# Optimization experiments

Measured on AMD Instinct MI355X. Metric: run time of the kernel, lower is better.

## Reference

```python
import jax, jax.numpy as jnp
import numpy as np

B, N, F_IN, F_OUT = 16, 2048, 512, 512


def setup_inputs() -> dict:
    key = jax.random.key(0)
    k1, k2, k3 = jax.random.split(key, 3)
    x = jax.random.normal(k1, (B, N, F_IN), dtype=jnp.float32)
    adj = jax.random.uniform(k2, (N, N), dtype=jnp.float32)
    # Kaiming uniform fan_out: bound = sqrt(6 / fan_out)
    bound = np.sqrt(6.0 / F_OUT)
    weight = jax.random.uniform(k3, (F_IN, F_OUT), dtype=jnp.float32,
                                minval=-bound, maxval=bound)
    bias = jnp.zeros((F_OUT,), dtype=jnp.float32)
    return {"x": x, "adj": adj, "weight": weight, "bias": bias}


def reference(x, adj, weight, bias):
    # Symmetric degree normalization: D^{-1/2} A D^{-1/2}
    deg = adj.sum(axis=1)                                   # [N]
    deg_inv_sqrt = jnp.where(deg > 0, jax.lax.rsqrt(deg), 0.0)
    # row/column rescale instead of diag matmuls (same math, O(N^2))
    norm_adj = adj * deg_inv_sqrt[:, None] * deg_inv_sqrt[None, :]
    support = jnp.einsum('bni,io->bno', x, weight)          # [B,N,F_OUT]
    output = jnp.einsum('nm,bmo->bno', norm_adj, support)   # [B,N,F_OUT]
    return output + bias
```

## Files before the change

### kernel.cpp

```cpp
#include <hip/hip_runtime.h>
#include <stdint.h>

typedef __attribute__((ext_vector_type(8))) __bf16 bf16x8;
typedef __attribute__((ext_vector_type(4))) float f32x4;
typedef unsigned short u16;

__device__ __forceinline__ u16 f2bf(float f) {
  unsigned u = __builtin_bit_cast(unsigned, f);
  unsigned r = 0x7FFFu + ((u >> 16) & 1u);
  return (u16)((u + r) >> 16);
}

__device__ __forceinline__ void gload16(const void* g, void* l) {
  __builtin_amdgcn_global_load_lds(
      (__attribute__((address_space(1))) void*)(g),
      (__attribute__((address_space(3))) void*)(l),
      16, 0, 0);
}

__global__ void row_deg_k(const float* __restrict__ adj, float* __restrict__ dis, int N) {
  int row = blockIdx.x;
  const float4* a = (const float4*)(adj + (size_t)row * N);
  float s = 0.f;
  for (int j = threadIdx.x; j < N / 4; j += 256) {
    float4 v = a[j];
    s += v.x + v.y + v.z + v.w;
  }
#pragma unroll
  for (int off = 32; off > 0; off >>= 1) s += __shfl_down(s, off, 64);
  __shared__ float wsum[4];
  if ((threadIdx.x & 63) == 0) wsum[threadIdx.x >> 6] = s;
  __syncthreads();
  if (threadIdx.x == 0) {
    float t = wsum[0] + wsum[1] + wsum[2] + wsum[3];
    dis[row] = (t > 0.f) ? (1.0f / sqrtf(t)) : 0.f;
  }
}

__global__ void conv_bf16_k(const float* __restrict__ in, u16* __restrict__ o, int n4) {
  int i = blockIdx.x * 256 + threadIdx.x;
  if (i >= n4) return;
  float4 v = ((const float4*)in)[i];
  ushort4 u;
  u.x = f2bf(v.x); u.y = f2bf(v.y); u.z = f2bf(v.z); u.w = f2bf(v.w);
  ((ushort4*)o)[i] = u;
}

__global__ void conv_wt_k(const float* __restrict__ w, u16* __restrict__ wt) {
  int idx = blockIdx.x * 256 + threadIdx.x;
  int i = idx >> 9, o = idx & 511;
  wt[o * 512 + i] = f2bf(w[idx]);
}

__global__ void make_nadj_k(const float* __restrict__ adj, const float* __restrict__ dis,
                            u16* __restrict__ o, int N) {
  int idx = blockIdx.x * 256 + threadIdx.x;
  int i = idx >> 9;
  int j4 = (idx & 511) * 4;
  float di = dis[i];
  float4 a = ((const float4*)adj)[idx];
  ushort4 u;
  u.x = f2bf(a.x * di * dis[j4 + 0]);
  u.y = f2bf(a.y * di * dis[j4 + 1]);
  u.z = f2bf(a.z * di * dis[j4 + 2]);
  u.w = f2bf(a.w * di * dis[j4 + 3]);
  ((ushort4*)o)[idx] = u;
}

template <int EPI>
__launch_bounds__(512, 2)
__global__ void gemm256_k(const u16* __restrict__ A, int lda,
                          const u16* __restrict__ Bt, int ldb,
                          void* __restrict__ Cv, int ldc,
                          const float* __restrict__ bias, int K,
                          int nMT, int nNT, size_t zBt, size_t zC) {
  __shared__ __align__(16) u16 lds[65536];

  const int tid = threadIdx.x;
  const int lane = tid & 63;
  const int wid = tid >> 6;
  const int wr = wid >> 2;
  const int wc = wid & 3;

  const int flat = blockIdx.x;
  const int wg = (flat & 7) * ((int)gridDim.x >> 3) + (flat >> 3);
  const int m_t = wg % nMT;
  const int rest = wg / nMT;
  const int n_t = rest % nNT;
  const int b = rest / nNT;
  const int rowBase = m_t * 256;
  const int colBase = n_t * 256;
  const u16* Bb = Bt + (size_t)b * zBt;

  const int lr = tid >> 3;
  const int kkl = (tid & 7) * 8;
  const int kswz = kkl ^ ((lr & 7) << 3);
  const u16* gA = A + (size_t)(rowBase + lr) * lda + kswz;
  const u16* gB = Bb + (size_t)(colBase + lr) * ldb + kswz;
  u16* lA = lds + lr * 64 + kkl;
  u16* lB = lds + 32768 + lr * 64 + kkl;

  const int fr = lane & 15;
  const int rswz = (lane & 7) << 3;
  const int kp0 = ((lane >> 4) * 8) ^ rswz;
  const int kp1 = (32 | ((lane >> 4) * 8)) ^ rswz;
  const u16* fA = lds + (wr * 128 + fr) * 64;
  const u16* fB = lds + 32768 + (wc * 64 + fr) * 64;

  f32x4 acc[8][4] = {};

  const int NT = K >> 6;

#define STAGE_ALL(d, t)                                                              \
  _Pragma("unroll") for (int r4 = 0; r4 < 4; ++r4) {                                 \
    gload16(gA + (size_t)(r4 * 64) * lda + (size_t)(t) * 64,                         \
            lA + (d) * 16384 + r4 * 4096);                                           \
    gload16(gB + (size_t)(r4 * 64) * ldb + (size_t)(t) * 64,                         \
            lB + (d) * 16384 + r4 * 4096);                                           \
  }

  STAGE_ALL(0, 0);
  __syncthreads();

  for (int t = 0; t < NT; ++t) {
    const int c = t & 1;
    const int cn = c ^ 1;
    const int tn = (t + 1 < NT) ? t + 1 : NT - 1;

    STAGE_ALL(cn, tn);
    __builtin_amdgcn_sched_barrier(0);

    bf16x8 a0[8], a1[8], b0[4], b1[4];
#pragma unroll
    for (int m = 0; m < 8; ++m) {
      a0[m] = *(const bf16x8*)(fA + c * 16384 + m * 1024 + kp0);
      a1[m] = *(const bf16x8*)(fA + c * 16384 + m * 1024 + kp1);
    }
#pragma unroll
    for (int n = 0; n < 4; ++n) {
      b0[n] = *(const bf16x8*)(fB + c * 16384 + n * 1024 + kp0);
      b1[n] = *(const bf16x8*)(fB + c * 16384 + n * 1024 + kp1);
    }
#pragma unroll
    for (int m = 0; m < 8; ++m)
#pragma unroll
      for (int n = 0; n < 4; ++n)
        acc[m][n] = __builtin_amdgcn_mfma_f32_16x16x32_bf16(a0[m], b0[n], acc[m][n], 0, 0, 0);
#pragma unroll
    for (int m = 0; m < 8; ++m)
#pragma unroll
      for (int n = 0; n < 4; ++n)
        acc[m][n] = __builtin_amdgcn_mfma_f32_16x16x32_bf16(a1[m], b1[n], acc[m][n], 0, 0, 0);

    __syncthreads();
  }

  if (EPI == 0) {
    u16* C = (u16*)Cv;
#pragma unroll
    for (int m = 0; m < 8; ++m) {
      const int r = rowBase + wr * 128 + m * 16 + (lane >> 4) * 4;
#pragma unroll
      for (int n = 0; n < 4; ++n) {
        const int cc = colBase + wc * 64 + n * 16 + (lane & 15);
        ushort4 v;
        v.x = f2bf(acc[m][n][0]);
        v.y = f2bf(acc[m][n][1]);
        v.z = f2bf(acc[m][n][2]);
        v.w = f2bf(acc[m][n][3]);
        *reinterpret_cast<ushort4*>(&C[(size_t)cc * ldc + r]) = v;
      }
    }
  } else {
    float* C = (float*)Cv + (size_t)b * zC;
#pragma unroll
    for (int n = 0; n < 4; ++n) {
      const int cc = colBase + wc * 64 + n * 16 + (lane & 15);
      const float bv = bias[cc];
#pragma unroll
      for (int m = 0; m < 8; ++m) {
        const int r = rowBase + wr * 128 + m * 16 + (lane >> 4) * 4;
#pragma unroll
        for (int j = 0; j < 4; ++j)
          C[(size_t)(r + j) * ldc + cc] = acc[m][n][j] + bv;
      }
    }
  }
#undef STAGE_ALL
}

extern "C" void kernel_launch(void* const* d_in, const int* in_sizes, int n_in,
                              void* d_out, int out_size, void* d_ws, size_t ws_size,
                              hipStream_t stream) {
  const int B = 16, N = 2048, FIN = 512, FOUT = 512;
  const float* x    = (const float*)d_in[0];
  const float* adj  = (const float*)d_in[1];
  const float* w    = (const float*)d_in[2];
  const float* bias = (const float*)d_in[3];
  float* out = (float*)d_out;
  char* ws = (char*)d_ws;

  float* dis = (float*)ws;
  u16* wt    = (u16*)(ws + 8192);
  u16* nadj  = (u16*)(ws + 532480);
  u16* xb    = (u16*)(ws + 8921088);
  u16* st    = (u16*)(ws + 42475520);

  row_deg_k<<<N, 256, 0, stream>>>(adj, dis, N);
  conv_bf16_k<<<(B * N * FIN / 4 + 255) / 256, 256, 0, stream>>>(x, xb, B * N * FIN / 4);
  conv_wt_k<<<(FIN * FOUT) / 256, 256, 0, stream>>>(w, wt);
  make_nadj_k<<<(N * N / 4) / 256, 256, 0, stream>>>(adj, dis, nadj, N);

  gemm256_k<0><<<dim3(256), 512, 0, stream>>>(
      xb, FIN, wt, FIN, st, B * N, nullptr, FIN, 128, 2, 0, 0);

  gemm256_k<1><<<dim3(256), 512, 0, stream>>>(
      nadj, N, st, B * N, out, FOUT, bias, N, 8, 2,
      (size_t)N, (size_t)N * FOUT);
}
```

Baseline: 124.6 us.

## Fuse x fp32-to-bf16 conversion into first GEMM and retile second GEMM

The separate x-to-bf16 conversion kernel is removed. The first GEMM now loads fp32 x through registers, converts it with the hardware bf16 conversion, and writes swizzled tiles to LDS, which saves a full write and re-read of the bf16 copy of x. The second GEMM uses 128-row tiles with single-buffered, smaller LDS, twice as many blocks, and higher occupancy (launch bounds 512,4). The cost is that it drops the double-buffered prefetch, so it now relies on occupancy to hide load latency.

```diff
diff --git a/kernel.cpp b/kernel.cpp
--- a/kernel.cpp
+++ b/kernel.cpp
@@ -1,4 +1,5 @@
 #include <hip/hip_runtime.h>
+#include <hip/hip_bf16.h>
 #include <stdint.h>
 
 typedef __attribute__((ext_vector_type(8))) __bf16 bf16x8;
@@ -9,6 +10,11 @@
   unsigned u = __builtin_bit_cast(unsigned, f);
   unsigned r = 0x7FFFu + ((u >> 16) & 1u);
   return (u16)((u + r) >> 16);
+}
+
+__device__ __forceinline__ u16 f2bf_hw(float f) {
+  __hip_bfloat16 h = __float2bfloat16(f);
+  return __builtin_bit_cast(u16, h);
 }
 
 __device__ __forceinline__ void gload16(const void* g, void* l) {
@@ -35,15 +41,6 @@
     float t = wsum[0] + wsum[1] + wsum[2] + wsum[3];
     dis[row] = (t > 0.f) ? (1.0f / sqrtf(t)) : 0.f;
   }
-}
-
-__global__ void conv_bf16_k(const float* __restrict__ in, u16* __restrict__ o, int n4) {
-  int i = blockIdx.x * 256 + threadIdx.x;
-  if (i >= n4) return;
-  float4 v = ((const float4*)in)[i];
-  ushort4 u;
-  u.x = f2bf(v.x); u.y = f2bf(v.y); u.z = f2bf(v.z); u.w = f2bf(v.w);
-  ((ushort4*)o)[i] = u;
 }
 
 __global__ void conv_wt_k(const float* __restrict__ w, u16* __restrict__ wt) {
@@ -67,13 +64,10 @@
   ((ushort4*)o)[idx] = u;
 }
 
-template <int EPI>
 __launch_bounds__(512, 2)
-__global__ void gemm256_k(const u16* __restrict__ A, int lda,
-                          const u16* __restrict__ Bt, int ldb,
-                          void* __restrict__ Cv, int ldc,
-                          const float* __restrict__ bias, int K,
-                          int nMT, int nNT, size_t zBt, size_t zC) {
+__global__ void gemm1_xw_k(const float* __restrict__ X,
+                           const u16* __restrict__ Wt,
+                           u16* __restrict__ Ct, int M) {
   __shared__ __align__(16) u16 lds[65536];
 
   const int tid = threadIdx.x;
@@ -83,12 +77,136 @@
   const int wc = wid & 3;
 
   const int flat = blockIdx.x;
-  const int wg = (flat & 7) * ((int)gridDim.x >> 3) + (flat >> 3);
+  const int wg = (flat & 7) * 32 + (flat >> 3);
+  const int m_t = wg & 127;
+  const int n_t = wg >> 7;
+  const int rowBase = m_t * 256;
+  const int colBase = n_t * 256;
+
+  const int lr = tid >> 3;
+  const int kkl = (tid & 7) * 8;
+  const int s = (lr & 7) << 3;
+  const int kswz = kkl ^ s;
+  const float* gX = X + (size_t)(rowBase + lr) * 512 + kkl;
+  const u16* gB = Wt + (size_t)(colBase + lr) * 512 + kswz;
+  u16* lAsw = lds + lr * 64 + kswz;
+  u16* lB = lds + 32768 + lr * 64 + kkl;
+
+  const int fr = lane & 15;
+  const int rswz = (lane & 7) << 3;
+  const int kp0 = ((lane >> 4) * 8) ^ rswz;
+  const int kp1 = (32 | ((lane >> 4) * 8)) ^ rswz;
+  const u16* fA = lds + (wr * 128 + fr) * 64;
+  const u16* fB = lds + 32768 + (wc * 64 + fr) * 64;
+
+  f32x4 acc[8][4] = {};
+  f32x4 xv[4][2];
+
+  const int NT = 8;
+
+#define LOADX(t)                                                                     \
+  _Pragma("unroll") for (int r4 = 0; r4 < 4; ++r4) {                                 \
+    xv[r4][0] = *(const f32x4*)(gX + (size_t)(r4 * 64) * 512 + (t) * 64);            \
+    xv[r4][1] = *(const f32x4*)(gX + (size_t)(r4 * 64) * 512 + (t) * 64 + 4);        \
+  }
+
+#define STAGE_B1(d, t)                                                               \
+  _Pragma("unroll") for (int r4 = 0; r4 < 4; ++r4)                                   \
+    gload16(gB + (size_t)(r4 * 64) * 512 + (size_t)(t) * 64,                         \
+            lB + (d) * 16384 + r4 * 4096);
+
+#define WRITE_A(d)                                                                   \
+  _Pragma("unroll") for (int r4 = 0; r4 < 4; ++r4) {                                 \
+    bf16x8 v;                                                                        \
+    _Pragma("unroll") for (int i = 0; i < 4; ++i) {                                  \
+      v[i] = __builtin_bit_cast(__bf16, f2bf_hw(xv[r4][0][i]));                      \
+      v[4 + i] = __builtin_bit_cast(__bf16, f2bf_hw(xv[r4][1][i]));                  \
+    }                                                                                \
+    *(bf16x8*)(lAsw + (d) * 16384 + r4 * 4096) = v;                                  \
+  }
+
+  LOADX(0);
+  STAGE_B1(0, 0);
+  WRITE_A(0);
+  __syncthreads();
+
+  for (int t = 0; t < NT; ++t) {
+    const int c = t & 1;
+    const int cn = c ^ 1;
+    const int tn = (t + 1 < NT) ? t + 1 : NT - 1;
+
+    LOADX(tn);
+    STAGE_B1(cn, tn);
+    __builtin_amdgcn_sched_barrier(0);
+
+    bf16x8 a0[8], a1[8], b0[4], b1[4];
+#pragma unroll
+    for (int m = 0; m < 8; ++m) {
+      a0[m] = *(const bf16x8*)(fA + c * 16384 + m * 1024 + kp0);
+      a1[m] = *(const bf16x8*)(fA + c * 16384 + m * 1024 + kp1);
+    }
+#pragma unroll
+    for (int n = 0; n < 4; ++n) {
+      b0[n] = *(const bf16x8*)(fB + c * 16384 + n * 1024 + kp0);
+      b1[n] = *(const bf16x8*)(fB + c * 16384 + n * 1024 + kp1);
+    }
+#pragma unroll
+    for (int m = 0; m < 8; ++m)
+#pragma unroll
+      for (int n = 0; n < 4; ++n)
+        acc[m][n] = __builtin_amdgcn_mfma_f32_16x16x32_bf16(a0[m], b0[n], acc[m][n], 0, 0, 0);
+#pragma unroll
+    for (int m = 0; m < 8; ++m)
+#pragma unroll
+      for (int n = 0; n < 4; ++n)
+        acc[m][n] = __builtin_amdgcn_mfma_f32_16x16x32_bf16(a1[m], b1[n], acc[m][n], 0, 0, 0);
+
+    __builtin_amdgcn_sched_barrier(0);
+    WRITE_A(cn);
+    __syncthreads();
+  }
+
+#pragma unroll
+  for (int m = 0; m < 8; ++m) {
+    const int r = rowBase + wr * 128 + m * 16 + (lane >> 4) * 4;
+#pragma unroll
+    for (int n = 0; n < 4; ++n) {
+      const int cc = colBase + wc * 64 + n * 16 + (lane & 15);
+      ushort4 v;
+      v.x = f2bf(acc[m][n][0]);
+      v.y = f2bf(acc[m][n][1]);
+      v.z = f2bf(acc[m][n][2]);
+      v.w = f2bf(acc[m][n][3]);
+      *reinterpret_cast<ushort4*>(&Ct[(size_t)cc * M + r]) = v;
+    }
+  }
+#undef LOADX
+#undef STAGE_B1
+#undef WRITE_A
+}
+
+__launch_bounds__(512, 4)
+__global__ void gemm2b_k(const u16* __restrict__ A, int lda,
+                         const u16* __restrict__ Bt, int ldb,
+                         float* __restrict__ C, int ldc,
+                         const float* __restrict__ bias, int K,
+                         int nMT, int nNT, size_t zBt, size_t zC) {
+  __shared__ __align__(16) u16 lds[24576];
+
+  const int tid = threadIdx.x;
+  const int lane = tid & 63;
+  const int wid = tid >> 6;
+  const int wr = wid >> 2;
+  const int wc = wid & 3;
+
+  const int flat = blockIdx.x;
+  const int cpx = (int)gridDim.x >> 3;
+  const int wg = (flat & 7) * cpx + (flat >> 3);
   const int m_t = wg % nMT;
   const int rest = wg / nMT;
   const int n_t = rest % nNT;
   const int b = rest / nNT;
-  const int rowBase = m_t * 256;
+  const int rowBase = m_t * 128;
   const int colBase = n_t * 256;
   const u16* Bb = Bt + (size_t)b * zBt;
 
@@ -98,95 +216,62 @@
   const u16* gA = A + (size_t)(rowBase + lr) * lda + kswz;
   const u16* gB = Bb + (size_t)(colBase + lr) * ldb + kswz;
   u16* lA = lds + lr * 64 + kkl;
-  u16* lB = lds + 32768 + lr * 64 + kkl;
+  u16* lB = lds + 8192 + lr * 64 + kkl;
 
   const int fr = lane & 15;
   const int rswz = (lane & 7) << 3;
   const int kp0 = ((lane >> 4) * 8) ^ rswz;
   const int kp1 = (32 | ((lane >> 4) * 8)) ^ rswz;
-  const u16* fA = lds + (wr * 128 + fr) * 64;
-  const u16* fB = lds + 32768 + (wc * 64 + fr) * 64;
-
-  f32x4 acc[8][4] = {};
-
+  const u16* fA = lds + (wr * 64 + fr) * 64;
+  const u16* fB = lds + 8192 + (wc * 64 + fr) * 64;
+
+  f32x4 acc[4][4] = {};
   const int NT = K >> 6;
 
-#define STAGE_ALL(d, t)                                                              \
-  _Pragma("unroll") for (int r4 = 0; r4 < 4; ++r4) {                                 \
-    gload16(gA + (size_t)(r4 * 64) * lda + (size_t)(t) * 64,                         \
-            lA + (d) * 16384 + r4 * 4096);                                           \
-    gload16(gB + (size_t)(r4 * 64) * ldb + (size_t)(t) * 64,                         \
-            lB + (d) * 16384 + r4 * 4096);                                           \
-  }
-
-  STAGE_ALL(0, 0);
-  __syncthreads();
-
   for (int t = 0; t < NT; ++t) {
-    const int c = t & 1;
-    const int cn = c ^ 1;
-    const int tn = (t + 1 < NT) ? t + 1 : NT - 1;
-
-    STAGE_ALL(cn, tn);
-    __builtin_amdgcn_sched_barrier(0);
-
-    bf16x8 a0[8], a1[8], b0[4], b1[4];
-#pragma unroll
-    for (int m = 0; m < 8; ++m) {
-      a0[m] = *(const bf16x8*)(fA + c * 16384 + m * 1024 + kp0);
-      a1[m] = *(const bf16x8*)(fA + c * 16384 + m * 1024 + kp1);
+    gload16(gA + (size_t)t * 64, lA);
+    gload16(gA + (size_t)64 * lda + (size_t)t * 64, lA + 4096);
+#pragma unroll
+    for (int r4 = 0; r4 < 4; ++r4)
+      gload16(gB + (size_t)(r4 * 64) * ldb + (size_t)t * 64, lB + r4 * 4096);
+    __syncthreads();
+
+    bf16x8 a[4], bb[4];
+#pragma unroll
+    for (int m = 0; m < 4; ++m) a[m] = *(const bf16x8*)(fA + m * 1024 + kp0);
+#pragma unroll
+    for (int n = 0; n < 4; ++n) bb[n] = *(const bf16x8*)(fB + n * 1024 + kp0);
+#pragma unroll
+    for (int m = 0; m < 4; ++m)
+#pragma unroll
+      for (int n = 0; n < 4; ++n)
+        acc[m][n] = __builtin_amdgcn_mfma_f32_16x16x32_bf16(a[m], bb[n], acc[m][n], 0, 0, 0);
+#pragma unroll
+    for (int m = 0; m < 4; ++m) a[m] = *(const bf16x8*)(fA + m * 1024 + kp1);
+#pragma unroll
+    for (int n = 0; n < 4; ++n) bb[n] = *(const bf16x8*)(fB + n * 1024 + kp1);
+#pragma unroll
+    for (int m = 0; m < 4; ++m)
+#pragma unroll
+      for (int n = 0; n < 4; ++n)
+        acc[m][n] = __builtin_amdgcn_mfma_f32_16x16x32_bf16(a[m], bb[n], acc[m][n], 0, 0, 0);
+
+    __syncthreads();
+  }
+
+  float* Cb = C + (size_t)b * zC;
+#pragma unroll
+  for (int n = 0; n < 4; ++n) {
+    const int cc = colBase + wc * 64 + n * 16 + (lane & 15);
+    const float bv = bias[cc];
+#pragma unroll
+    for (int m = 0; m < 4; ++m) {
+      const int r = rowBase + wr * 64 + m * 16 + (lane >> 4) * 4;
+#pragma unroll
+      for (int j = 0; j < 4; ++j)
+        Cb[(size_t)(r + j) * ldc + cc] = acc[m][n][j] + bv;
     }
-#pragma unroll
-    for (int n = 0; n < 4; ++n) {
-      b0[n] = *(const bf16x8*)(fB + c * 16384 + n * 1024 + kp0);
-      b1[n] = *(const bf16x8*)(fB + c * 16384 + n * 1024 + kp1);
-    }
-#pragma unroll
-    for (int m = 0; m < 8; ++m)
-#pragma unroll
-      for (int n = 0; n < 4; ++n)
-        acc[m][n] = __builtin_amdgcn_mfma_f32_16x16x32_bf16(a0[m], b0[n], acc[m][n], 0, 0, 0);
-#pragma unroll
-    for (int m = 0; m < 8; ++m)
-#pragma unroll
-      for (int n = 0; n < 4; ++n)
-        acc[m][n] = __builtin_amdgcn_mfma_f32_16x16x32_bf16(a1[m], b1[n], acc[m][n], 0, 0, 0);
-
-    __syncthreads();
-  }
-
-  if (EPI == 0) {
-    u16* C = (u16*)Cv;
-#pragma unroll
-    for (int m = 0; m < 8; ++m) {
-      const int r = rowBase + wr * 128 + m * 16 + (lane >> 4) * 4;
-#pragma unroll
-      for (int n = 0; n < 4; ++n) {
-        const int cc = colBase + wc * 64 + n * 16 + (lane & 15);
-        ushort4 v;
-        v.x = f2bf(acc[m][n][0]);
-        v.y = f2bf(acc[m][n][1]);
-        v.z = f2bf(acc[m][n][2]);
-        v.w = f2bf(acc[m][n][3]);
-        *reinterpret_cast<ushort4*>(&C[(size_t)cc * ldc + r]) = v;
-      }
-    }
-  } else {
-    float* C = (float*)Cv + (size_t)b * zC;
-#pragma unroll
-    for (int n = 0; n < 4; ++n) {
-      const int cc = colBase + wc * 64 + n * 16 + (lane & 15);
-      const float bv = bias[cc];
-#pragma unroll
-      for (int m = 0; m < 8; ++m) {
-        const int r = rowBase + wr * 128 + m * 16 + (lane >> 4) * 4;
-#pragma unroll
-        for (int j = 0; j < 4; ++j)
-          C[(size_t)(r + j) * ldc + cc] = acc[m][n][j] + bv;
-      }
-    }
-  }
-#undef STAGE_ALL
+  }
 }
 
 extern "C" void kernel_launch(void* const* d_in, const int* in_sizes, int n_in,
@@ -203,18 +288,15 @@
   float* dis = (float*)ws;
   u16* wt    = (u16*)(ws + 8192);
   u16* nadj  = (u16*)(ws + 532480);
-  u16* xb    = (u16*)(ws + 8921088);
-  u16* st    = (u16*)(ws + 42475520);
+  u16* st    = (u16*)(ws + 8921088);
 
   row_deg_k<<<N, 256, 0, stream>>>(adj, dis, N);
-  conv_bf16_k<<<(B * N * FIN / 4 + 255) / 256, 256, 0, stream>>>(x, xb, B * N * FIN / 4);
   conv_wt_k<<<(FIN * FOUT) / 256, 256, 0, stream>>>(w, wt);
   make_nadj_k<<<(N * N / 4) / 256, 256, 0, stream>>>(adj, dis, nadj, N);
 
-  gemm256_k<0><<<dim3(256), 512, 0, stream>>>(
-      xb, FIN, wt, FIN, st, B * N, nullptr, FIN, 128, 2, 0, 0);
-
-  gemm256_k<1><<<dim3(256), 512, 0, stream>>>(
-      nadj, N, st, B * N, out, FOUT, bias, N, 8, 2,
+  gemm1_xw_k<<<dim3(256), 512, 0, stream>>>(x, wt, st, B * N);
+
+  gemm2b_k<<<dim3(512), 512, 0, stream>>>(
+      nadj, N, st, B * N, out, FOUT, bias, N, 16, 2,
       (size_t)N, (size_t)N * FOUT);
 }
```

Measured after the change: 115.9 us. -7.0%, faster.
